# Kernel optimization log

Hardware: AMD Instinct MI355X
Metric: run time of the kernel (lower is better)

The kernel has to match this reference:

```python
import jax, jax.numpy as jnp
import numpy as np

VOCAB = 50001  # vocab_size + 1
EMB = 64
HID = 128
TAGS = 32
B, T = 256, 512


def setup_inputs() -> dict:
    key = jax.random.key(0)
    ks = jax.random.split(key, 12)
    inputs = jax.random.randint(ks[0], (B, T), 0, VOCAB)
    labels = jax.random.randint(ks[1], (B, T), 0, TAGS)
    E = jax.random.normal(ks[2], (VOCAB, EMB), jnp.float32) * 0.1
    def glorot(k, shape):
        fan = sum(shape)
        return jax.random.uniform(k, shape, jnp.float32, -1.0, 1.0) * jnp.sqrt(6.0 / fan)
    Wk_f = glorot(ks[3], (EMB, 4 * HID))
    Wr_f = glorot(ks[4], (HID, 4 * HID))
    b_f = jnp.zeros((4 * HID,), jnp.float32)
    Wk_b = glorot(ks[5], (EMB, 4 * HID))
    Wr_b = glorot(ks[6], (HID, 4 * HID))
    b_b = jnp.zeros((4 * HID,), jnp.float32)
    Wd = glorot(ks[7], (2 * HID, TAGS))
    bd = jnp.zeros((TAGS,), jnp.float32)
    transition = jax.random.uniform(ks[8], (TAGS, TAGS), jnp.float32)
    return {"inputs": inputs, "labels": labels, "E": E,
            "Wk_f": Wk_f, "Wr_f": Wr_f, "b_f": b_f,
            "Wk_b": Wk_b, "Wr_b": Wr_b, "b_b": b_b,
            "Wd": Wd, "bd": bd, "transition": transition}


def _lstm(x, Wk, Wr, b, reverse):
    # x: (B, T, D) -> (B, T, H); Keras gate order i, f, g(cell), o
    Bb = x.shape[0]
    H = Wr.shape[0]
    xs = jnp.swapaxes(x, 0, 1)  # (T, B, D)

    def step(carry, xt):
        h, c = carry
        z = xt @ Wk + h @ Wr + b
        i, f, g, o = jnp.split(z, 4, axis=-1)
        c = jax.nn.sigmoid(f) * c + jax.nn.sigmoid(i) * jnp.tanh(g)
        h = jax.nn.sigmoid(o) * jnp.tanh(c)
        return (h, c), h

    init = (jnp.zeros((Bb, H), x.dtype), jnp.zeros((Bb, H), x.dtype))
    _, hs = jax.lax.scan(step, init, xs, reverse=reverse)
    return jnp.swapaxes(hs, 0, 1)  # (B, T, H), time-aligned for both directions


def _crf_log_likelihood(logits, labels, transition):
    # logits: (B, T, K), labels: (B, T) int, full-length sequences
    lt = jnp.swapaxes(logits, 0, 1)  # (T, B, K)

    def fstep(alpha, lg):
        # alpha: (B, K) -> logsumexp over previous tag
        alpha = jax.nn.logsumexp(alpha[:, :, None] + transition[None], axis=1) + lg
        return alpha, None

    alpha, _ = jax.lax.scan(fstep, lt[0], lt[1:])
    log_norm = jax.nn.logsumexp(alpha, axis=-1)  # (B,)
    unary = jnp.take_along_axis(logits, labels[..., None], axis=-1)[..., 0].sum(-1)
    binary = transition[labels[:, :-1], labels[:, 1:]].sum(-1)
    return unary + binary - log_norm


def reference(inputs, labels, E, Wk_f, Wr_f, b_f, Wk_b, Wr_b, b_b, Wd, bd, transition):
    emb = E[inputs]  # (B, T, EMB) embedding lookup
    h_f = _lstm(emb, Wk_f, Wr_f, b_f, reverse=False)
    h_b = _lstm(emb, Wk_b, Wr_b, b_b, reverse=True)
    h = jnp.concatenate([h_f, h_b], axis=-1)  # (B, T, 2H)
    logits = h @ Wd + bd  # (B, T, K)
    log_likelihood = _crf_log_likelihood(logits, labels, transition)
    return log_likelihood, transition
```

## Files before the change

### kernel.cpp

```cpp
#include <hip/hip_runtime.h>
#include <hip/hip_bf16.h>
#include <cstdint>
#include <cstddef>

#define VOCAB 50001
#define EMB 64
#define HID 128
#define G4  512
#define TAGS 32
#define BATCH 256
#define SEQ 512

typedef _Float16 f16;
typedef _Float16 f16x2 __attribute__((ext_vector_type(2)));
typedef _Float16 f16x4 __attribute__((ext_vector_type(4)));
typedef _Float16 f16x8 __attribute__((ext_vector_type(8)));
typedef float f32x4 __attribute__((ext_vector_type(4)));

__device__ __forceinline__ float rcpf(float x) { return __builtin_amdgcn_rcpf(x); }
__device__ __forceinline__ float rfl(float x) {
  return __builtin_bit_cast(float, __builtin_amdgcn_readfirstlane(__builtin_bit_cast(int, x)));
}

#define MFMA16(A, B, C) __builtin_amdgcn_mfma_f32_16x16x32_f16((A), (B), (C), 0, 0, 0)

__global__ __launch_bounds__(256)
void gtab_mfma_kernel(const float* __restrict__ E,
                      const float* __restrict__ Wk_f, const float* __restrict__ b_f,
                      const float* __restrict__ Wk_b, const float* __restrict__ b_b,
                      f16* __restrict__ G_f, f16* __restrict__ G_b) {
  const int dir = blockIdx.z;
  const float* __restrict__ Wk   = dir ? Wk_b : Wk_f;
  const float* __restrict__ bias = dir ? b_b  : b_f;
  f16* __restrict__ G = dir ? G_b : G_f;

  const int m0 = blockIdx.x * 64;
  const int n0 = blockIdx.y * 256;
  const int tid = threadIdx.x;

  __shared__ f16 Eh[64][80];
  __shared__ f16 Bh[256][80];

  #pragma unroll
  for (int s = 0; s < 4; ++s) {
    int idx = tid + s * 256;
    int r = idx >> 4, c4 = (idx & 15) * 4;
    int row = m0 + r;
    float4 ev;
    if (row < VOCAB) ev = *(const float4*)(E + (size_t)row * EMB + c4);
    else { ev.x = 0.f; ev.y = 0.f; ev.z = 0.f; ev.w = 0.f; }
    f16x4 v; v[0] = (f16)ev.x; v[1] = (f16)ev.y; v[2] = (f16)ev.z; v[3] = (f16)ev.w;
    *(f16x4*)&Eh[r][c4] = v;
  }
  #pragma unroll
  for (int s = 0; s < 32; ++s) {
    int idx = tid + s * 256;
    int k = idx >> 7, n2 = (idx & 127) * 2;
    float2 wv = *(const float2*)(Wk + (size_t)k * G4 + n0 + n2);
    Bh[n2][k]     = (f16)wv.x;
    Bh[n2 + 1][k] = (f16)wv.y;
  }
  __syncthreads();

  const int w = tid >> 6, l = tid & 63, mn = l & 15, q = l >> 4;
  f16x8 a0 = *(const f16x8*)&Eh[16 * w + mn][8 * q];
  f16x8 a1 = *(const f16x8*)&Eh[16 * w + mn][32 + 8 * q];

  f32x4 acc[16];
  #pragma unroll
  for (int nt = 0; nt < 16; ++nt) {
    f16x8 b0 = *(const f16x8*)&Bh[16 * nt + mn][8 * q];
    f16x8 b1 = *(const f16x8*)&Bh[16 * nt + mn][32 + 8 * q];
    f32x4 z = {0.f, 0.f, 0.f, 0.f};
    z = MFMA16(a0, b0, z);
    z = MFMA16(a1, b1, z);
    acc[nt] = z;
  }

  const int gA = n0 >> 7;
  #pragma unroll
  for (int nt = 0; nt < 8; ++nt) {
    int hid = 16 * nt + mn;
    float bv0 = bias[n0 + 16 * nt + mn];
    float bv1 = bias[n0 + 128 + 16 * nt + mn];
    #pragma unroll
    for (int reg = 0; reg < 4; ++reg) {
      int row = m0 + 16 * w + 4 * q + reg;
      if (row < VOCAB) {
        f16x2 v; v.x = (f16)(acc[nt][reg] + bv0); v.y = (f16)(acc[nt + 8][reg] + bv1);
        *(f16x2*)(G + (size_t)row * G4 + hid * 4 + gA) = v;
      }
    }
  }
}

__global__ __launch_bounds__(512, 1)
void lstm_mfma_kernel(const int* __restrict__ tokens,
                      const f16* __restrict__ G_f, const f16* __restrict__ G_b,
                      const float* __restrict__ Wr_f, const float* __restrict__ Wr_b,
                      const float* __restrict__ Wd, const float* __restrict__ bd,
                      float* __restrict__ Lf, float* __restrict__ Lb) {
  const int bg  = blockIdx.x;
  const int dir = blockIdx.y;
  const int b0  = bg * 4;
  const f16* __restrict__ G = dir ? G_b : G_f;
  const char* __restrict__ Gc = (const char*)G;
  const float* __restrict__ Wr = dir ? Wr_b : Wr_f;
  float* __restrict__ Lout = dir ? Lb : Lf;

  const int tid = threadIdx.x;
  const int w = tid >> 6;
  const int l = tid & 63;
  const int mn = l & 15;
  const int q  = l >> 4;
  const int hid = 16 * w + mn;
  const int hid8 = hid * 8;

  __shared__ __align__(16) f16 h_lds[2][4][160];
  __shared__ int tokT[SEQ][4];

  #pragma unroll
  for (int s = 0; s < 4; ++s) {
    int idx = tid + s * 512;
    int t = idx >> 2, qq = idx & 3;
    tokT[t][qq] = tokens[(size_t)(b0 + qq) * SEQ + t] << 10;
  }
  if (tid < 320) ((unsigned*)&h_lds[0][0][0])[tid] = 0u;

  f16x8 bw[4][4];
  #pragma unroll
  for (int g = 0; g < 4; ++g) {
    #pragma unroll
    for (int s = 0; s < 4; ++s) {
      f16x8 v;
      const int colv = 128 * g + hid;
      #pragma unroll
      for (int j = 0; j < 8; ++j)
        v[j] = (f16)Wr[(size_t)(32 * s + 8 * q + j) * G4 + colv];
      bw[g][s] = v;
    }
  }
  f16x8 wdf0{}, wdf1{}, wdf2{}, wdf3{};
  float bdv = 0.0f;
  if (w >= 6) {
    const int tag = 16 * (w - 6) + mn;
    #pragma unroll
    for (int j = 0; j < 8; ++j) {
      wdf0[j] = (f16)Wd[(size_t)(128 * dir +  0 + 8 * q + j) * TAGS + tag];
      wdf1[j] = (f16)Wd[(size_t)(128 * dir + 32 + 8 * q + j) * TAGS + tag];
      wdf2[j] = (f16)Wd[(size_t)(128 * dir + 64 + 8 * q + j) * TAGS + tag];
      wdf3[j] = (f16)Wd[(size_t)(128 * dir + 96 + 8 * q + j) * TAGS + tag];
    }
    if (dir == 0) bdv = bd[tag];
  }

  float cst = 0.0f;
  __syncthreads();

#define TT(S) (dir ? (SEQ - 1 - (S)) : (S))

#define LOADG(S, GV) do {                                                      \
    int _tk = tokT[TT(S)][q];                                                  \
    GV = *(const uint2*)(Gc + _tk + hid8);                                     \
  } while (0)

#define SEL4(V) ((q & 2) ? ((q & 1) ? V[3] : V[2]) : ((q & 1) ? V[1] : V[0]))

#define STEP(S, GV) do {                                                       \
    const int _s = (S);                                                        \
    const int _t = TT(_s);                                                     \
    const f16* hb = &h_lds[_s & 1][mn & 3][0];                                 \
    f16x8 a0 = *(const f16x8*)(hb      + 8 * q);                               \
    f16x8 a1 = *(const f16x8*)(hb + 32 + 8 * q);                               \
    f16x8 a2 = *(const f16x8*)(hb + 64 + 8 * q);                               \
    f16x8 a3 = *(const f16x8*)(hb + 96 + 8 * q);                               \
    f32x4 z0 = {0.f,0.f,0.f,0.f}, z1 = {0.f,0.f,0.f,0.f};                      \
    f32x4 z2 = {0.f,0.f,0.f,0.f}, z3 = {0.f,0.f,0.f,0.f};                      \
    z0 = MFMA16(a0, bw[0][0], z0); z0 = MFMA16(a1, bw[0][1], z0);              \
    z0 = MFMA16(a2, bw[0][2], z0); z0 = MFMA16(a3, bw[0][3], z0);              \
    z1 = MFMA16(a0, bw[1][0], z1); z1 = MFMA16(a1, bw[1][1], z1);              \
    z1 = MFMA16(a2, bw[1][2], z1); z1 = MFMA16(a3, bw[1][3], z1);              \
    z2 = MFMA16(a0, bw[2][0], z2); z2 = MFMA16(a1, bw[2][1], z2);              \
    z2 = MFMA16(a2, bw[2][2], z2); z2 = MFMA16(a3, bw[2][3], z2);              \
    z3 = MFMA16(a0, bw[3][0], z3); z3 = MFMA16(a1, bw[3][1], z3);              \
    z3 = MFMA16(a2, bw[3][2], z3); z3 = MFMA16(a3, bw[3][3], z3);              \
    if (w >= 6) {                                                              \
      f32x4 la = {0.f,0.f,0.f,0.f};                                            \
      la = MFMA16(a0, wdf0, la); la = MFMA16(a1, wdf1, la);                    \
      la = MFMA16(a2, wdf2, la); la = MFMA16(a3, wdf3, la);                    \
      if (q == 0) {                                                            \
        const int tag = 16 * (w - 6) + mn;                                     \
        Lout[((size_t)(b0 + 0) * SEQ + _t) * TAGS + tag] = la[0] + bdv;        \
        Lout[((size_t)(b0 + 1) * SEQ + _t) * TAGS + tag] = la[1] + bdv;        \
        Lout[((size_t)(b0 + 2) * SEQ + _t) * TAGS + tag] = la[2] + bdv;        \
        Lout[((size_t)(b0 + 3) * SEQ + _t) * TAGS + tag] = la[3] + bdv;        \
      }                                                                        \
    }                                                                          \
    {                                                                          \
      float zi = SEL4(z0);                                                     \
      float zf = SEL4(z1);                                                     \
      float zg = SEL4(z2);                                                     \
      float zo = SEL4(z3);                                                     \
      f16x4 gv = __builtin_bit_cast(f16x4, GV);                                \
      zi += (float)gv[0]; zf += (float)gv[1];                                  \
      zg += (float)gv[2]; zo += (float)gv[3];                                  \
      float ei = __expf(-zi);                                                  \
      float eg = __expf(fminf(2.f * zg, 30.f));                                \
      float sab = (eg - 1.f) * rcpf((1.f + ei) * (eg + 1.f));                  \
      float ef = __expf(-zf);                                                  \
      float cc = rcpf(1.f + ef) * cst + sab;                                   \
      cst = cc;                                                                \
      float eo = __expf(-zo);                                                  \
      float ec = __expf(fminf(2.f * cc, 30.f));                                \
      float hh = (ec - 1.f) * rcpf((1.f + eo) * (ec + 1.f));                   \
      h_lds[(_s + 1) & 1][q][hid] = (f16)hh;                                   \
    }                                                                          \
    asm volatile("s_waitcnt lgkmcnt(0)" ::: "memory");                         \
    __builtin_amdgcn_s_barrier();                                              \
  } while (0)

  uint2 gA, gB, gC, gD;
  LOADG(0, gA); LOADG(1, gB); LOADG(2, gC); LOADG(3, gD);

  for (int it = 0; it < SEQ / 4; ++it) {
    const int s = 4 * it;
    STEP(s + 0, gA);
    { int sc = (s + 4 < SEQ) ? s + 4 : SEQ - 1; LOADG(sc, gA); }
    STEP(s + 1, gB);
    { int sc = (s + 5 < SEQ) ? s + 5 : SEQ - 1; LOADG(sc, gB); }
    STEP(s + 2, gC);
    { int sc = (s + 6 < SEQ) ? s + 6 : SEQ - 1; LOADG(sc, gC); }
    STEP(s + 3, gD);
    { int sc = (s + 7 < SEQ) ? s + 7 : SEQ - 1; LOADG(sc, gD); }
  }
#undef STEP
#undef SEL4
#undef LOADG
#undef TT
}

__global__ __launch_bounds__(64)
void crf_kernel(const float* __restrict__ Lf,
                const float* __restrict__ Lb,
                const float* __restrict__ trans,
                const int* __restrict__ labels,
                float* __restrict__ out) {
  const int b = blockIdx.x;
  const int lane = threadIdx.x;
  const int k  = lane & 31;
  const int jh = lane >> 5;

  __shared__ float tr[TAGS * TAGS];
  __shared__ __align__(16) float e_lds[TAGS];

  for (int i = lane; i < TAGS * TAGS; i += 64) tr[i] = trans[i];
  __syncthreads();

  float wxp[16];
  #pragma unroll
  for (int i = 0; i < 16; ++i) wxp[i] = __expf(tr[(jh * 16 + i) * TAGS + k]);

  const size_t base0 = (size_t)b * SEQ * TAGS;
  float cur = Lf[base0 + k] + Lb[base0 + k];
  float beta0 = rfl(cur);
  float beta = cur - beta0;
  float S = beta0;

  float nxt = Lf[base0 + TAGS + k] + Lb[base0 + TAGS + k];

  for (int t = 1; t < SEQ; ++t) {
    float e = __expf(beta);
    if (lane < TAGS) e_lds[k] = e;
    asm volatile("s_waitcnt lgkmcnt(0)" ::: "memory");
    const float4* ep = (const float4*)&e_lds[jh * 16];
    float4 e0 = ep[0], e1 = ep[1], e2 = ep[2], e3 = ep[3];
    float d0 = e0.x * wxp[0]  + e0.y * wxp[1]  + e0.z * wxp[2]  + e0.w * wxp[3];
    float d1 = e1.x * wxp[4]  + e1.y * wxp[5]  + e1.z * wxp[6]  + e1.w * wxp[7];
    float d2 = e2.x * wxp[8]  + e2.y * wxp[9]  + e2.z * wxp[10] + e2.w * wxp[11];
    float d3 = e3.x * wxp[12] + e3.y * wxp[13] + e3.z * wxp[14] + e3.w * wxp[15];
    float dot = (d0 + d1) + (d2 + d3);
    dot += __shfl_xor(dot, 32);
    float braw = __logf(dot) + nxt;
    float bz = rfl(braw);
    beta = braw - bz;
    S += bz;
    if (t + 1 < SEQ) {
      size_t idx = base0 + (size_t)(t + 1) * TAGS + k;
      nxt = Lf[idx] + Lb[idx];
    }
  }

  float m = beta;
  #pragma unroll
  for (int off = 1; off <= 16; off <<= 1) m = fmaxf(m, __shfl_xor(m, off));
  float ex = (lane < TAGS) ? __expf(beta - m) : 0.0f;
  float s = ex;
  #pragma unroll
  for (int off = 1; off <= 32; off <<= 1) s += __shfl_xor(s, off);

  const int* lab = labels + (size_t)b * SEQ;
  float uacc = 0.f, bacc = 0.f;
  for (int t = lane; t < SEQ; t += 64) {
    int l0 = lab[t];
    size_t idx = base0 + (size_t)t * TAGS + l0;
    uacc += Lf[idx] + Lb[idx];
    if (t + 1 < SEQ) bacc += tr[l0 * TAGS + lab[t + 1]];
  }
  float red = uacc + bacc;
  #pragma unroll
  for (int off = 1; off <= 32; off <<= 1) red += __shfl_xor(red, off);

  if (lane == 0) out[b] = red - (m + __logf(s) + S);
}

__global__ void copy_trans_kernel(const float* __restrict__ trans,
                                  float* __restrict__ out) {
  int i = blockIdx.x * blockDim.x + threadIdx.x;
  if (i < TAGS * TAGS) out[i] = trans[i];
}

extern "C" void kernel_launch(void* const* d_in, const int* in_sizes, int n_in,
                              void* d_out, int out_size, void* d_ws, size_t ws_size,
                              hipStream_t stream) {
  const int*   inputs = (const int*)  d_in[0];
  const int*   labels = (const int*)  d_in[1];
  const float* E      = (const float*)d_in[2];
  const float* Wk_f   = (const float*)d_in[3];
  const float* Wr_f   = (const float*)d_in[4];
  const float* b_f    = (const float*)d_in[5];
  const float* Wk_b   = (const float*)d_in[6];
  const float* Wr_b   = (const float*)d_in[7];
  const float* b_b    = (const float*)d_in[8];
  const float* Wd     = (const float*)d_in[9];
  const float* bd     = (const float*)d_in[10];
  const float* trans  = (const float*)d_in[11];
  float* out = (float*)d_out;

  char* ws = (char*)d_ws;
  const size_t G_ELEMS = (size_t)VOCAB * G4;
  f16* G_f = (f16*)ws;
  f16* G_b = G_f + G_ELEMS;
  float* Lfp = (float*)(ws + 2 * G_ELEMS * sizeof(f16));
  float* Lbp = Lfp + (size_t)BATCH * SEQ * TAGS;

  dim3 ggrid((VOCAB + 63) / 64, 2, 2);
  gtab_mfma_kernel<<<ggrid, 256, 0, stream>>>(E, Wk_f, b_f, Wk_b, b_b, G_f, G_b);

  lstm_mfma_kernel<<<dim3(BATCH / 4, 2), 512, 0, stream>>>(
      inputs, G_f, G_b, Wr_f, Wr_b, Wd, bd, Lfp, Lbp);

  crf_kernel<<<BATCH, 64, 0, stream>>>(Lfp, Lbp, trans, labels, out);

  copy_trans_kernel<<<(TAGS * TAGS + 255) / 256, 256, 0, stream>>>(trans, out + BATCH);
}
```

Measured before the change: 513.6 us.

## Loop gate-table N halves per block, use pointer-stepped logit stores, renormalize CRF less often

The gate-table kernel now handles both 256-column halves of Wk in one block instead of launching a separate block per half. This halves the grid and reuses the staged embedding tile, at the cost of serialized work per block and extra barriers. The LSTM logit stores and CRF logit loads now step running pointers instead of recomputing full indices each step. The CRF forward pass renormalizes via readfirstlane only every fourth step, which shortens the serial chain but lets beta drift further before exp, a small overflow risk.

```diff
diff --git a/kernel.cpp b/kernel.cpp
--- a/kernel.cpp
+++ b/kernel.cpp
@@ -35,7 +35,6 @@
   f16* __restrict__ G = dir ? G_b : G_f;
 
   const int m0 = blockIdx.x * 64;
-  const int n0 = blockIdx.y * 256;
   const int tid = threadIdx.x;
 
   __shared__ f16 Eh[64][80];
@@ -52,45 +51,56 @@
     f16x4 v; v[0] = (f16)ev.x; v[1] = (f16)ev.y; v[2] = (f16)ev.z; v[3] = (f16)ev.w;
     *(f16x4*)&Eh[r][c4] = v;
   }
-  #pragma unroll
-  for (int s = 0; s < 32; ++s) {
-    int idx = tid + s * 256;
-    int k = idx >> 7, n2 = (idx & 127) * 2;
-    float2 wv = *(const float2*)(Wk + (size_t)k * G4 + n0 + n2);
-    Bh[n2][k]     = (f16)wv.x;
-    Bh[n2 + 1][k] = (f16)wv.y;
-  }
-  __syncthreads();
 
   const int w = tid >> 6, l = tid & 63, mn = l & 15, q = l >> 4;
-  f16x8 a0 = *(const f16x8*)&Eh[16 * w + mn][8 * q];
-  f16x8 a1 = *(const f16x8*)&Eh[16 * w + mn][32 + 8 * q];
-
-  f32x4 acc[16];
-  #pragma unroll
-  for (int nt = 0; nt < 16; ++nt) {
-    f16x8 b0 = *(const f16x8*)&Bh[16 * nt + mn][8 * q];
-    f16x8 b1 = *(const f16x8*)&Bh[16 * nt + mn][32 + 8 * q];
-    f32x4 z = {0.f, 0.f, 0.f, 0.f};
-    z = MFMA16(a0, b0, z);
-    z = MFMA16(a1, b1, z);
-    acc[nt] = z;
-  }
-
-  const int gA = n0 >> 7;
-  #pragma unroll
-  for (int nt = 0; nt < 8; ++nt) {
-    int hid = 16 * nt + mn;
-    float bv0 = bias[n0 + 16 * nt + mn];
-    float bv1 = bias[n0 + 128 + 16 * nt + mn];
-    #pragma unroll
-    for (int reg = 0; reg < 4; ++reg) {
-      int row = m0 + 16 * w + 4 * q + reg;
-      if (row < VOCAB) {
-        f16x2 v; v.x = (f16)(acc[nt][reg] + bv0); v.y = (f16)(acc[nt + 8][reg] + bv1);
-        *(f16x2*)(G + (size_t)row * G4 + hid * 4 + gA) = v;
+  f16x8 a0, a1;
+  bool afrag_loaded = false;
+
+  for (int np = 0; np < 2; ++np) {
+    const int n0 = np * 256;
+    #pragma unroll
+    for (int s = 0; s < 32; ++s) {
+      int idx = tid + s * 256;
+      int k = idx >> 7, n2 = (idx & 127) * 2;
+      float2 wv = *(const float2*)(Wk + (size_t)k * G4 + n0 + n2);
+      Bh[n2][k]     = (f16)wv.x;
+      Bh[n2 + 1][k] = (f16)wv.y;
+    }
+    __syncthreads();
+
+    if (!afrag_loaded) {
+      a0 = *(const f16x8*)&Eh[16 * w + mn][8 * q];
+      a1 = *(const f16x8*)&Eh[16 * w + mn][32 + 8 * q];
+      afrag_loaded = true;
+    }
+
+    f32x4 acc[16];
+    #pragma unroll
+    for (int nt = 0; nt < 16; ++nt) {
+      f16x8 b0 = *(const f16x8*)&Bh[16 * nt + mn][8 * q];
+      f16x8 b1 = *(const f16x8*)&Bh[16 * nt + mn][32 + 8 * q];
+      f32x4 z = {0.f, 0.f, 0.f, 0.f};
+      z = MFMA16(a0, b0, z);
+      z = MFMA16(a1, b1, z);
+      acc[nt] = z;
+    }
+
+    const int gA = n0 >> 7;
+    #pragma unroll
+    for (int nt = 0; nt < 8; ++nt) {
+      int hid = 16 * nt + mn;
+      float bv0 = bias[n0 + 16 * nt + mn];
+      float bv1 = bias[n0 + 128 + 16 * nt + mn];
+      #pragma unroll
+      for (int reg = 0; reg < 4; ++reg) {
+        int row = m0 + 16 * w + 4 * q + reg;
+        if (row < VOCAB) {
+          f16x2 v; v.x = (f16)(acc[nt][reg] + bv0); v.y = (f16)(acc[nt + 8][reg] + bv1);
+          *(f16x2*)(G + (size_t)row * G4 + hid * 4 + gA) = v;
+        }
       }
     }
+    __syncthreads();
   }
 }
 
@@ -154,6 +164,11 @@
     if (dir == 0) bdv = bd[tag];
   }
 
+  const int t0 = dir ? (SEQ - 1) : 0;
+  const int tagw = (w >= 6) ? (16 * (w - 6) + mn) : 0;
+  char* lp = (char*)(Lout + ((size_t)b0 * SEQ + t0) * TAGS + tagw);
+  const int ldt = dir ? -(int)(TAGS * 4) : (int)(TAGS * 4);
+
   float cst = 0.0f;
   __syncthreads();
 
@@ -168,7 +183,6 @@
 
 #define STEP(S, GV) do {                                                       \
     const int _s = (S);                                                        \
-    const int _t = TT(_s);                                                     \
     const f16* hb = &h_lds[_s & 1][mn & 3][0];                                 \
     f16x8 a0 = *(const f16x8*)(hb      + 8 * q);                               \
     f16x8 a1 = *(const f16x8*)(hb + 32 + 8 * q);                               \
@@ -189,13 +203,13 @@
       la = MFMA16(a0, wdf0, la); la = MFMA16(a1, wdf1, la);                    \
       la = MFMA16(a2, wdf2, la); la = MFMA16(a3, wdf3, la);                    \
       if (q == 0) {                                                            \
-        const int tag = 16 * (w - 6) + mn;                                     \
-        Lout[((size_t)(b0 + 0) * SEQ + _t) * TAGS + tag] = la[0] + bdv;        \
-        Lout[((size_t)(b0 + 1) * SEQ + _t) * TAGS + tag] = la[1] + bdv;        \
-        Lout[((size_t)(b0 + 2) * SEQ + _t) * TAGS + tag] = la[2] + bdv;        \
-        Lout[((size_t)(b0 + 3) * SEQ + _t) * TAGS + tag] = la[3] + bdv;        \
+        *(float*)(lp               ) = la[0] + bdv;                            \
+        *(float*)(lp + SEQ*TAGS*4  ) = la[1] + bdv;                            \
+        *(float*)(lp + SEQ*TAGS*8  ) = la[2] + bdv;                            \
+        *(float*)(lp + SEQ*TAGS*12 ) = la[3] + bdv;                            \
       }                                                                        \
     }                                                                          \
+    lp += ldt;                                                                 \
     {                                                                          \
       float zi = SEL4(z0);                                                     \
       float zf = SEL4(z1);                                                     \
@@ -266,7 +280,9 @@
   float beta = cur - beta0;
   float S = beta0;
 
-  float nxt = Lf[base0 + TAGS + k] + Lb[base0 + TAGS + k];
+  const float* lfp = Lf + base0 + TAGS + k;
+  const float* lbp = Lb + base0 + TAGS + k;
+  float nxt = *lfp + *lbp;
 
   for (int t = 1; t < SEQ; ++t) {
     float e = __expf(beta);
@@ -281,12 +297,16 @@
     float dot = (d0 + d1) + (d2 + d3);
     dot += __shfl_xor(dot, 32);
     float braw = __logf(dot) + nxt;
-    float bz = rfl(braw);
-    beta = braw - bz;
-    S += bz;
+    if ((t & 3) == 0) {
+      float bz = rfl(braw);
+      beta = braw - bz;
+      S += bz;
+    } else {
+      beta = braw;
+    }
     if (t + 1 < SEQ) {
-      size_t idx = base0 + (size_t)(t + 1) * TAGS + k;
-      nxt = Lf[idx] + Lb[idx];
+      lfp += TAGS; lbp += TAGS;
+      nxt = *lfp + *lbp;
     }
   }
 
@@ -343,7 +363,7 @@
   float* Lfp = (float*)(ws + 2 * G_ELEMS * sizeof(f16));
   float* Lbp = Lfp + (size_t)BATCH * SEQ * TAGS;
 
-  dim3 ggrid((VOCAB + 63) / 64, 2, 2);
+  dim3 ggrid((VOCAB + 63) / 64, 1, 2);
   gtab_mfma_kernel<<<ggrid, 256, 0, stream>>>(E, Wk_f, b_f, Wk_b, b_b, G_f, G_b);
 
   lstm_mfma_kernel<<<dim3(BATCH / 4, 2), 512, 0, stream>>>(
```

Result: slower. 602.9 us (+17.4%).
